# Kernel optimization log

Measured on AMD Instinct MI355X. Metric: run time of the kernel, lower is better.

Reference implementation:

```python
import jax, jax.numpy as jnp
from jax import lax
import numpy as np

KW = 9
PAD = KW // 2  # 4, matches int(kernel_width/2) with stride-1 'same' conv


def _scnn_dir(x, w, b):
    """Sequential SCNN scan over axis 1 of x (shape [N, S, W, C]).
    Each step: cur = relu(conv1d_along_C(prev)) + x[:, i], out[0] = x[:, 0].
    conv is cross-correlation with kernel w (shape [KW]) + scalar bias b,
    matching nn.Conv2d(1, 1, kernel_size=(1, KW), padding=(0, PAD)).
    """
    k = w.reshape(1, 1, 1, KW)  # OIHW-style kernel: out=1, in=1, (1, KW)

    def conv(prev):  # prev: [N, W, C]
        y = lax.conv_general_dilated(prev[:, None, :, :], k,
                                     window_strides=(1, 1),
                                     padding=((0, 0), (PAD, PAD)))
        return y[:, 0] + b  # [N, W, C]

    xt = jnp.moveaxis(x, 1, 0)  # [S, N, W, C]

    def step(prev, xi):
        cur = jax.nn.relu(conv(prev)) + xi
        return cur, cur

    _, rest = lax.scan(step, xt[0], xt[1:])
    out = jnp.concatenate([xt[:1], rest], axis=0)
    return jnp.moveaxis(out, 0, 1)  # [N, S, W, C]


def setup_inputs() -> dict:
    key = jax.random.key(0)
    ks = jax.random.split(key, 9)
    N, C, H, W = 8, 128, 160, 160
    x = jax.random.normal(ks[0], (N, C, H, W), dtype=jnp.float32)
    scale = 1.0 / np.sqrt(KW)  # torch Conv2d default init scale (uniform bound)
    def wgt(k):
        return jax.random.uniform(k, (KW,), jnp.float32, -scale, scale)
    def bia(k):
        return jax.random.uniform(k, (), jnp.float32, -scale, scale)
    return {
        "x": x,
        "w_d": wgt(ks[1]), "b_d": bia(ks[2]),
        "w_u": wgt(ks[3]), "b_u": bia(ks[4]),
        "w_l": wgt(ks[5]), "b_l": bia(ks[6]),
        "w_r": wgt(ks[7]), "b_r": bia(ks[8]),
    }


def reference(x, w_d, b_d, w_u, b_u, w_l, b_l, w_r, b_r):
    out = jnp.transpose(x, (0, 2, 3, 1))                 # NCHW -> NHWC, scan over H (down)
    out = jax.nn.relu(_scnn_dir(out, w_d, b_d))
    out = jnp.flip(out, axis=1)                          # up direction
    out = jax.nn.relu(_scnn_dir(out, w_u, b_u))
    out = jnp.transpose(out, (0, 2, 1, 3))               # scan over W (left)
    out = jax.nn.relu(_scnn_dir(out, w_l, b_l))
    out = jnp.flip(out, axis=1)                          # right direction
    out = jax.nn.relu(_scnn_dir(out, w_r, b_r))
    return jnp.transpose(out, (0, 3, 2, 1))              # back to NCHW
```

## Files before the change

kernel.cpp:

```cpp
#include <hip/hip_runtime.h>

#define NB 8
#define CH 128
#define HH 160
#define WW 160
#define SPILL 100
#define LDS_ROWS 60

__device__ __forceinline__ float dpp_up1(float x) {
    return __int_as_float(__builtin_amdgcn_update_dpp(0, __float_as_int(x), 0x138, 0xF, 0xF, true));
}
__device__ __forceinline__ float dpp_dn1(float x) {
    return __int_as_float(__builtin_amdgcn_update_dpp(0, __float_as_int(x), 0x130, 0xF, 0xF, true));
}

__device__ __forceinline__ float2 conv9(float2 p, const float* w, float b) {
    float m1x = dpp_up1(p.x), m1y = dpp_up1(p.y);
    float m2x = dpp_up1(m1x), m2y = dpp_up1(m1y);
    float p1x = dpp_dn1(p.x), p1y = dpp_dn1(p.y);
    float p2x = dpp_dn1(p1x), p2y = dpp_dn1(p1y);
    float e0=m2x,e1=m2y,e2=m1x,e3=m1y,e4=p.x,e5=p.y,e6=p1x,e7=p1y,e8=p2x,e9=p2y;
    float ax = fmaf(w[0], e0, b);       ax = fmaf(w[3], e3, ax); ax = fmaf(w[6], e6, ax);
    float bx = w[1]*e1;                 bx = fmaf(w[4], e4, bx); bx = fmaf(w[7], e7, bx);
    float cx = w[2]*e2;                 cx = fmaf(w[5], e5, cx); cx = fmaf(w[8], e8, cx);
    float ay = fmaf(w[0], e1, b);       ay = fmaf(w[3], e4, ay); ay = fmaf(w[6], e7, ay);
    float by = w[1]*e2;                 by = fmaf(w[4], e5, by); by = fmaf(w[7], e8, by);
    float cy = w[2]*e3;                 cy = fmaf(w[5], e6, cy); cy = fmaf(w[8], e9, cy);
    return make_float2((ax + bx) + cx, (ay + by) + cy);
}

__global__ __launch_bounds__(256) void k0_transpose(const float* __restrict__ x,
                                                    float* __restrict__ A) {
    __shared__ float t[32][132];
    int p0 = blockIdx.x * 128;
    int c0 = blockIdx.y * 32;
    int n  = blockIdx.z;
    int tid = threadIdx.x;
    const float* xn = x + (size_t)n * CH * HH * WW;
    float* An = A + (size_t)n * HH * WW * CH;
    #pragma unroll
    for (int j = 0; j < 4; j++) {
        int c = j*8 + tid/32;
        int q4 = (tid%32)*4;
        float4 v = *(const float4*)(xn + (size_t)(c0 + c) * (HH*WW) + p0 + q4);
        *(float4*)&t[c][q4] = v;
    }
    __syncthreads();
    #pragma unroll
    for (int j = 0; j < 8; j++) {
        int p  = j*16 + tid/16;
        int cq = (tid%16)*2;
        float2 v = make_float2(t[cq][p], t[cq+1][p]);
        *(float2*)(An + (size_t)(p0 + p) * CH + c0 + cq) = v;
    }
}

__global__ __launch_bounds__(64) void k1_vert(float* __restrict__ A,
        const float* __restrict__ wdp, const float* __restrict__ bdp,
        const float* __restrict__ wup, const float* __restrict__ bup) {
    __shared__ float lds[LDS_ROWS][CH];
    int lane = threadIdx.x;
    int w = blockIdx.x, n = blockIdx.y;
    float wd[9], wu[9];
    #pragma unroll
    for (int j = 0; j < 9; j++) { wd[j] = wdp[j]; wu[j] = wup[j]; }
    float bd = bdp[0], bu = bup[0];
    float* col = A + ((size_t)n * HH * WW + w) * CH + 2*lane;
    const size_t RS = (size_t)WW * CH;

    float2 d;
    float2 qf[16];
    #pragma unroll
    for (int i = 0; i < 16; i++) qf[i] = *(const float2*)(col + (size_t)i * RS);
    for (int hb = 0; hb < HH; hb += 16) {
        #pragma unroll
        for (int k = 0; k < 16; k++) {
            int h = hb + k;
            float2 xr = qf[k];
            if (h + 16 < HH) qf[k] = *(const float2*)(col + (size_t)(h+16) * RS);
            if (h == 0) d = xr;
            else {
                float2 cv = conv9(d, wd, bd);
                d.x = fmaxf(cv.x, 0.f) + xr.x;
                d.y = fmaxf(cv.y, 0.f) + xr.y;
            }
            float rx = fmaxf(d.x, 0.f), ry = fmaxf(d.y, 0.f);
            if (h < SPILL) *(float2*)(col + (size_t)h * RS) = make_float2(rx, ry);
            else { lds[h-SPILL][lane] = rx; lds[h-SPILL][64+lane] = ry; }
        }
    }

    float2 u;
    float2 tf[16];
    #pragma unroll
    for (int k = 0; k < 16; k++) {
        int h = HH - 1 - k;
        tf[k] = make_float2(lds[h-SPILL][lane], lds[h-SPILL][64+lane]);
    }
    for (int sb = 0; sb < HH; sb += 16) {
        #pragma unroll
        for (int k = 0; k < 16; k++) {
            int s = sb + k;
            int h = HH - 1 - s;
            float2 t2 = tf[k];
            int h2 = h - 16;
            if (h2 >= SPILL)    tf[k] = make_float2(lds[h2-SPILL][lane], lds[h2-SPILL][64+lane]);
            else if (h2 >= 0)   tf[k] = *(const float2*)(col + (size_t)h2 * RS);
            if (s == 0) u = t2;
            else {
                float2 cv = conv9(u, wu, bu);
                u.x = fmaxf(cv.x, 0.f) + t2.x;
                u.y = fmaxf(cv.y, 0.f) + t2.y;
            }
            *(float2*)(col + (size_t)h * RS) = u;
        }
    }
}

__global__ __launch_bounds__(64) void k2_horz(float* __restrict__ A,
        const float* __restrict__ wlp, const float* __restrict__ blp,
        const float* __restrict__ wrp, const float* __restrict__ brp,
        float* __restrict__ out) {
    __shared__ float lds[LDS_ROWS][CH];
    int lane = threadIdx.x;
    int hp = blockIdx.x, n = blockIdx.y;
    float wl[9], wr[9];
    #pragma unroll
    for (int j = 0; j < 9; j++) { wl[j] = wlp[j]; wr[j] = wrp[j]; }
    float bl = blp[0], br = brp[0];
    float* row0 = A + ((size_t)n * HH + hp) * WW * CH + 2*lane;
    const size_t PS = CH;

    float2 l;
    float2 qf[16];
    #pragma unroll
    for (int i = 0; i < 16; i++) qf[i] = *(const float2*)(row0 + (size_t)i * PS);
    for (int ab = 0; ab < WW; ab += 16) {
        #pragma unroll
        for (int k = 0; k < 16; k++) {
            int a = ab + k;
            float2 xr = qf[k];
            if (a + 16 < WW) qf[k] = *(const float2*)(row0 + (size_t)(a+16) * PS);
            xr.x = fmaxf(xr.x, 0.f); xr.y = fmaxf(xr.y, 0.f);
            if (a == 0) l = xr;
            else {
                float2 cv = conv9(l, wl, bl);
                l.x = fmaxf(cv.x, 0.f) + xr.x;
                l.y = fmaxf(cv.y, 0.f) + xr.y;
            }
            float rx = fmaxf(l.x, 0.f), ry = fmaxf(l.y, 0.f);
            if (a < SPILL) *(float2*)(row0 + (size_t)a * PS) = make_float2(rx, ry);
            else {
                int r = a - SPILL;
                int sw = r & 31;
                lds[r][lane ^ sw] = rx;
                lds[r][64 + (lane ^ sw)] = ry;
            }
        }
    }

    float2 u;
    float2 tf[16];
    #pragma unroll
    for (int k = 0; k < 16; k++) {
        int a = WW - 1 - k;
        int r = a - SPILL;
        int sw = r & 31;
        tf[k] = make_float2(lds[r][lane ^ sw], lds[r][64 + (lane ^ sw)]);
    }
    int ho  = HH - 1 - hp;
    int l31 = lane & 31;
    int hi  = lane >> 5;
    float* ob = out + ((size_t)(n * CH + hi) * HH + ho) * WW + l31;
    int jf = (179 - l31) % 60;
    int js = 59;

    for (int sb = 0; sb < WW; sb += 32) {
        #pragma unroll
        for (int kk = 0; kk < 32; kk++) {
            int s = sb + kk;
            int a = WW - 1 - s;
            float2 t6 = tf[kk & 15];
            int a2 = a - 16;
            if (a2 >= SPILL) {
                int r = a2 - SPILL;
                int sw = r & 31;
                tf[kk & 15] = make_float2(lds[r][lane ^ sw], lds[r][64 + (lane ^ sw)]);
            } else if (a2 >= 0) {
                tf[kk & 15] = *(const float2*)(row0 + (size_t)a2 * PS);
            }
            if (s == 0) u = t6;
            else {
                float2 cv = conv9(u, wr, br);
                u.x = fmaxf(cv.x, 0.f) + t6.x;
                u.y = fmaxf(cv.y, 0.f) + t6.y;
            }
            {
                int sw = js & 31;
                lds[js][lane ^ sw]        = fmaxf(u.x, 0.f);
                lds[js][64 + (lane ^ sw)] = fmaxf(u.y, 0.f);
            }
            js = js ? js - 1 : 59;
        }
        {
            int jx = jf & 31;
            int pl = jf * 128 + (hi << 6);
            const float* lp = &lds[0][0];
            #pragma unroll
            for (int i = 0; i < 64; i++) {
                float v = lp[pl + (i ^ jx)];
                ob[(size_t)(2*i) * (HH*WW) + sb] = v;
            }
            jf -= 32; if (jf < 0) jf += 60;
        }
    }
}

extern "C" void kernel_launch(void* const* d_in, const int* in_sizes, int n_in,
                              void* d_out, int out_size, void* d_ws, size_t ws_size,
                              hipStream_t stream) {
    (void)in_sizes; (void)n_in; (void)out_size; (void)ws_size;
    const float* x  = (const float*)d_in[0];
    const float* wd = (const float*)d_in[1];
    const float* bd = (const float*)d_in[2];
    const float* wu = (const float*)d_in[3];
    const float* bu = (const float*)d_in[4];
    const float* wl = (const float*)d_in[5];
    const float* bl = (const float*)d_in[6];
    const float* wr = (const float*)d_in[7];
    const float* br = (const float*)d_in[8];
    float* out = (float*)d_out;
    float* A   = (float*)d_ws;

    dim3 g0(HH*WW/128, CH/32, NB), b0(256);
    k0_transpose<<<g0, b0, 0, stream>>>(x, A);

    dim3 g1(WW, NB), b1(64);
    k1_vert<<<g1, b1, 0, stream>>>(A, wd, bd, wu, bu);

    dim3 g2(HH, NB);
    k2_horz<<<g2, b1, 0, stream>>>(A, wl, bl, wr, br, out);
}
```

Baseline: 332.1 us.

## Keep middle scan rows in registers, last rows in LDS to cut global traffic

Both scan kernels now keep rows 48-95 of the first-direction result in a 48-entry register array, rows 96-159 in a 64-row LDS buffer, and write only rows 0-47 to global memory. The reverse scan reads the register and LDS rows directly instead of round-tripping them through global memory, and prefetches the global rows it still needs. k2 reuses the LDS rows in place for the output transpose, with fixed flush points. Launch bounds now request two waves per SIMD, so the extra register pressure may cause spills or lower occupancy.

```diff
diff --git a/kernel.cpp b/kernel.cpp
--- a/kernel.cpp
+++ b/kernel.cpp
@@ -4,8 +4,6 @@
 #define CH 128
 #define HH 160
 #define WW 160
-#define SPILL 100
-#define LDS_ROWS 60
 
 __device__ __forceinline__ float dpp_up1(float x) {
     return __int_as_float(__builtin_amdgcn_update_dpp(0, __float_as_int(x), 0x138, 0xF, 0xF, true));
@@ -29,6 +27,12 @@
     return make_float2((ax + bx) + cx, (ay + by) + cy);
 }
 
+__device__ __forceinline__ void scan_step(float2& st, float2 xr, const float* w, float b) {
+    float2 cv = conv9(st, w, b);
+    st.x = fmaxf(cv.x, 0.f) + xr.x;
+    st.y = fmaxf(cv.y, 0.f) + xr.y;
+}
+
 __global__ __launch_bounds__(256) void k0_transpose(const float* __restrict__ x,
                                                     float* __restrict__ A) {
     __shared__ float t[32][132];
@@ -55,10 +59,10 @@
     }
 }
 
-__global__ __launch_bounds__(64) void k1_vert(float* __restrict__ A,
+__global__ __launch_bounds__(64, 2) void k1_vert(float* __restrict__ A,
         const float* __restrict__ wdp, const float* __restrict__ bdp,
         const float* __restrict__ wup, const float* __restrict__ bup) {
-    __shared__ float lds[LDS_ROWS][CH];
+    __shared__ float lds[64][CH];
     int lane = threadIdx.x;
     int w = blockIdx.x, n = blockIdx.y;
     float wd[9], wu[9];
@@ -69,149 +73,216 @@
     const size_t RS = (size_t)WW * CH;
 
     float2 d;
+    float2 rr[48];
     float2 qf[16];
     #pragma unroll
     for (int i = 0; i < 16; i++) qf[i] = *(const float2*)(col + (size_t)i * RS);
-    for (int hb = 0; hb < HH; hb += 16) {
+
+    for (int hb = 0; hb < 48; hb += 16) {
         #pragma unroll
         for (int k = 0; k < 16; k++) {
             int h = hb + k;
             float2 xr = qf[k];
+            qf[k] = *(const float2*)(col + (size_t)(h+16) * RS);
+            if (h == 0) d = xr;
+            else scan_step(d, xr, wd, bd);
+            *(float2*)(col + (size_t)h * RS) = make_float2(fmaxf(d.x,0.f), fmaxf(d.y,0.f));
+        }
+    }
+    #pragma unroll
+    for (int seg = 0; seg < 3; seg++) {
+        #pragma unroll
+        for (int k = 0; k < 16; k++) {
+            int h = 48 + seg*16 + k;
+            float2 xr = qf[k];
+            qf[k] = *(const float2*)(col + (size_t)(h+16) * RS);
+            scan_step(d, xr, wd, bd);
+            rr[seg*16 + k] = make_float2(fmaxf(d.x,0.f), fmaxf(d.y,0.f));
+        }
+    }
+    for (int hb = 96; hb < 160; hb += 16) {
+        #pragma unroll
+        for (int k = 0; k < 16; k++) {
+            int h = hb + k;
+            float2 xr = qf[k];
             if (h + 16 < HH) qf[k] = *(const float2*)(col + (size_t)(h+16) * RS);
-            if (h == 0) d = xr;
-            else {
-                float2 cv = conv9(d, wd, bd);
-                d.x = fmaxf(cv.x, 0.f) + xr.x;
-                d.y = fmaxf(cv.y, 0.f) + xr.y;
-            }
-            float rx = fmaxf(d.x, 0.f), ry = fmaxf(d.y, 0.f);
-            if (h < SPILL) *(float2*)(col + (size_t)h * RS) = make_float2(rx, ry);
-            else { lds[h-SPILL][lane] = rx; lds[h-SPILL][64+lane] = ry; }
+            scan_step(d, xr, wd, bd);
+            lds[h-96][lane]    = fmaxf(d.x,0.f);
+            lds[h-96][64+lane] = fmaxf(d.y,0.f);
         }
     }
 
     float2 u;
-    float2 tf[16];
-    #pragma unroll
-    for (int k = 0; k < 16; k++) {
-        int h = HH - 1 - k;
-        tf[k] = make_float2(lds[h-SPILL][lane], lds[h-SPILL][64+lane]);
-    }
-    for (int sb = 0; sb < HH; sb += 16) {
-        #pragma unroll
-        for (int k = 0; k < 16; k++) {
-            int s = sb + k;
-            int h = HH - 1 - s;
-            float2 t2 = tf[k];
+    float2 gq[16];
+    for (int sb = 0; sb < 64; sb += 16) {
+        #pragma unroll
+        for (int k = 0; k < 16; k++) {
+            int s = sb + k, h = 159 - s, r = h - 96;
+            float2 t2 = make_float2(lds[r][lane], lds[r][64+lane]);
+            if (sb == 0 && k == 0) u = t2;
+            else scan_step(u, t2, wu, bu);
+            *(float2*)(col + (size_t)h * RS) = u;
+        }
+    }
+    #pragma unroll
+    for (int seg = 0; seg < 3; seg++) {
+        #pragma unroll
+        for (int k = 0; k < 16; k++) {
+            int h = 95 - seg*16 - k;
+            float2 t2 = rr[h - 48];
+            scan_step(u, t2, wu, bu);
+            *(float2*)(col + (size_t)h * RS) = u;
+            if (seg == 0) gq[k] = *(const float2*)(col + (size_t)(47-k) * RS);
+        }
+    }
+    for (int sb = 112; sb < 160; sb += 16) {
+        #pragma unroll
+        for (int k = 0; k < 16; k++) {
+            int s = sb + k, h = 159 - s;
+            float2 t2 = gq[k];
             int h2 = h - 16;
-            if (h2 >= SPILL)    tf[k] = make_float2(lds[h2-SPILL][lane], lds[h2-SPILL][64+lane]);
-            else if (h2 >= 0)   tf[k] = *(const float2*)(col + (size_t)h2 * RS);
-            if (s == 0) u = t2;
-            else {
-                float2 cv = conv9(u, wu, bu);
-                u.x = fmaxf(cv.x, 0.f) + t2.x;
-                u.y = fmaxf(cv.y, 0.f) + t2.y;
-            }
+            if (h2 >= 0) gq[k] = *(const float2*)(col + (size_t)h2 * RS);
+            scan_step(u, t2, wu, bu);
             *(float2*)(col + (size_t)h * RS) = u;
         }
     }
 }
 
-__global__ __launch_bounds__(64) void k2_horz(float* __restrict__ A,
+__global__ __launch_bounds__(64, 2) void k2_horz(float* __restrict__ A,
         const float* __restrict__ wlp, const float* __restrict__ blp,
         const float* __restrict__ wrp, const float* __restrict__ brp,
         float* __restrict__ out) {
-    __shared__ float lds[LDS_ROWS][CH];
+    __shared__ float lds[64][CH];
     int lane = threadIdx.x;
     int hp = blockIdx.x, n = blockIdx.y;
-    float wl[9], wr[9];
-    #pragma unroll
-    for (int j = 0; j < 9; j++) { wl[j] = wlp[j]; wr[j] = wrp[j]; }
-    float bl = blp[0], br = brp[0];
+    float wA[9], wB[9];
+    #pragma unroll
+    for (int j = 0; j < 9; j++) { wA[j] = wlp[j]; wB[j] = wrp[j]; }
+    float bA = blp[0], bB = brp[0];
     float* row0 = A + ((size_t)n * HH + hp) * WW * CH + 2*lane;
     const size_t PS = CH;
 
     float2 l;
+    float2 rr[48];
     float2 qf[16];
     #pragma unroll
     for (int i = 0; i < 16; i++) qf[i] = *(const float2*)(row0 + (size_t)i * PS);
-    for (int ab = 0; ab < WW; ab += 16) {
+
+    for (int ab = 0; ab < 48; ab += 16) {
+        #pragma unroll
+        for (int k = 0; k < 16; k++) {
+            int a = ab + k;
+            float2 xr = qf[k];
+            qf[k] = *(const float2*)(row0 + (size_t)(a+16) * PS);
+            xr.x = fmaxf(xr.x, 0.f); xr.y = fmaxf(xr.y, 0.f);
+            if (a == 0) l = xr;
+            else scan_step(l, xr, wA, bA);
+            *(float2*)(row0 + (size_t)a * PS) = make_float2(fmaxf(l.x,0.f), fmaxf(l.y,0.f));
+        }
+    }
+    #pragma unroll
+    for (int seg = 0; seg < 3; seg++) {
+        #pragma unroll
+        for (int k = 0; k < 16; k++) {
+            int a = 48 + seg*16 + k;
+            float2 xr = qf[k];
+            qf[k] = *(const float2*)(row0 + (size_t)(a+16) * PS);
+            xr.x = fmaxf(xr.x, 0.f); xr.y = fmaxf(xr.y, 0.f);
+            scan_step(l, xr, wA, bA);
+            rr[seg*16 + k] = make_float2(fmaxf(l.x,0.f), fmaxf(l.y,0.f));
+        }
+    }
+    for (int ab = 96; ab < 160; ab += 16) {
         #pragma unroll
         for (int k = 0; k < 16; k++) {
             int a = ab + k;
             float2 xr = qf[k];
             if (a + 16 < WW) qf[k] = *(const float2*)(row0 + (size_t)(a+16) * PS);
             xr.x = fmaxf(xr.x, 0.f); xr.y = fmaxf(xr.y, 0.f);
-            if (a == 0) l = xr;
-            else {
-                float2 cv = conv9(l, wl, bl);
-                l.x = fmaxf(cv.x, 0.f) + xr.x;
-                l.y = fmaxf(cv.y, 0.f) + xr.y;
-            }
-            float rx = fmaxf(l.x, 0.f), ry = fmaxf(l.y, 0.f);
-            if (a < SPILL) *(float2*)(row0 + (size_t)a * PS) = make_float2(rx, ry);
-            else {
-                int r = a - SPILL;
-                int sw = r & 31;
-                lds[r][lane ^ sw] = rx;
-                lds[r][64 + (lane ^ sw)] = ry;
-            }
+            scan_step(l, xr, wA, bA);
+            int r = a - 96, sw = r & 31;
+            lds[r][lane ^ sw]        = fmaxf(l.x,0.f);
+            lds[r][64 + (lane ^ sw)] = fmaxf(l.y,0.f);
         }
     }
 
     float2 u;
-    float2 tf[16];
-    #pragma unroll
-    for (int k = 0; k < 16; k++) {
-        int a = WW - 1 - k;
-        int r = a - SPILL;
-        int sw = r & 31;
-        tf[k] = make_float2(lds[r][lane ^ sw], lds[r][64 + (lane ^ sw)]);
-    }
+    float2 gq[16];
     int ho  = HH - 1 - hp;
     int l31 = lane & 31;
     int hi  = lane >> 5;
     float* ob = out + ((size_t)(n * CH + hi) * HH + ho) * WW + l31;
-    int jf = (179 - l31) % 60;
-    int js = 59;
-
-    for (int sb = 0; sb < WW; sb += 32) {
-        #pragma unroll
-        for (int kk = 0; kk < 32; kk++) {
-            int s = sb + kk;
-            int a = WW - 1 - s;
-            float2 t6 = tf[kk & 15];
+    int jx = 31 - l31;
+    const float* lp = &lds[0][0];
+
+    for (int sb = 0; sb < 64; sb += 16) {
+        #pragma unroll
+        for (int k = 0; k < 16; k++) {
+            int s = sb + k, r = 63 - s, sw = r & 31;
+            int ci = lane ^ sw;
+            float2 t2 = make_float2(lds[r][ci], lds[r][64+ci]);
+            if (sb == 0 && k == 0) u = t2;
+            else scan_step(u, t2, wB, bB);
+            lds[r][ci]    = fmaxf(u.x, 0.f);
+            lds[r][64+ci] = fmaxf(u.y, 0.f);
+        }
+        if (sb == 16 || sb == 48) {
+            int jf = (sb == 16 ? 63 : 31) - l31;
+            int pl = jf*128 + (hi << 6);
+            int so = sb - 16;
+            #pragma unroll
+            for (int i = 0; i < 64; i++)
+                ob[(size_t)(2*i) * (HH*WW) + so] = lp[pl + (i ^ jx)];
+        }
+    }
+    #pragma unroll
+    for (int seg = 0; seg < 3; seg++) {
+        #pragma unroll
+        for (int k = 0; k < 16; k++) {
+            int s = 64 + seg*16 + k;
+            int a = 159 - s;
+            float2 t2 = rr[a - 48];
+            scan_step(u, t2, wB, bB);
+            int js = 63 - 16*seg - k;
+            int sw = js & 31;
+            lds[js][lane ^ sw]        = fmaxf(u.x, 0.f);
+            lds[js][64 + (lane ^ sw)] = fmaxf(u.y, 0.f);
+            if (seg == 0) gq[k] = *(const float2*)(row0 + (size_t)(47-k) * PS);
+        }
+        if (seg == 1) {
+            int jf = 63 - l31;
+            int pl = jf*128 + (hi << 6);
+            #pragma unroll
+            for (int i = 0; i < 64; i++)
+                ob[(size_t)(2*i) * (HH*WW) + 64] = lp[pl + (i ^ jx)];
+        }
+    }
+    for (int sb = 112; sb < 160; sb += 16) {
+        #pragma unroll
+        for (int k = 0; k < 16; k++) {
+            int s = sb + k, a = 159 - s;
+            float2 t2 = gq[k];
             int a2 = a - 16;
-            if (a2 >= SPILL) {
-                int r = a2 - SPILL;
-                int sw = r & 31;
-                tf[kk & 15] = make_float2(lds[r][lane ^ sw], lds[r][64 + (lane ^ sw)]);
-            } else if (a2 >= 0) {
-                tf[kk & 15] = *(const float2*)(row0 + (size_t)a2 * PS);
-            }
-            if (s == 0) u = t6;
-            else {
-                float2 cv = conv9(u, wr, br);
-                u.x = fmaxf(cv.x, 0.f) + t6.x;
-                u.y = fmaxf(cv.y, 0.f) + t6.y;
-            }
-            {
-                int sw = js & 31;
-                lds[js][lane ^ sw]        = fmaxf(u.x, 0.f);
-                lds[js][64 + (lane ^ sw)] = fmaxf(u.y, 0.f);
-            }
-            js = js ? js - 1 : 59;
-        }
-        {
-            int jx = jf & 31;
-            int pl = jf * 128 + (hi << 6);
-            const float* lp = &lds[0][0];
+            if (a2 >= 0) gq[k] = *(const float2*)(row0 + (size_t)a2 * PS);
+            scan_step(u, t2, wB, bB);
+            int js = 63 - (s & 63);
+            int sw = js & 31;
+            lds[js][lane ^ sw]        = fmaxf(u.x, 0.f);
+            lds[js][64 + (lane ^ sw)] = fmaxf(u.y, 0.f);
+        }
+        if (sb == 112) {
+            int jf = 31 - l31;
+            int pl = jf*128 + (hi << 6);
             #pragma unroll
-            for (int i = 0; i < 64; i++) {
-                float v = lp[pl + (i ^ jx)];
-                ob[(size_t)(2*i) * (HH*WW) + sb] = v;
-            }
-            jf -= 32; if (jf < 0) jf += 60;
+            for (int i = 0; i < 64; i++)
+                ob[(size_t)(2*i) * (HH*WW) + 96] = lp[pl + (i ^ jx)];
+        }
+        if (sb == 144) {
+            int jf = 63 - l31;
+            int pl = jf*128 + (hi << 6);
+            #pragma unroll
+            for (int i = 0; i < 64; i++)
+                ob[(size_t)(2*i) * (HH*WW) + 128] = lp[pl + (i ^ jx)];
         }
     }
 }
```

Result: slower. 593.3 us (+78.6%).

## Split vertical scan channels across two wavefronts with LDS halo exchange

Applied to the files above, without the earlier changes.

The vertical (down/up) scan kernel now uses 128 threads, one channel per thread across two wavefronts, instead of 64 threads each holding two channels. The 9-tap convolution across the wavefront boundary is completed with a small double-buffered LDS halo of 4 values per side, which needs a __syncthreads every row. The intent is to shorten the per-step serial dependency chain and double parallelism in the latency-bound sequential scan. The cost is a block-wide barrier on every one of the 320 steps, plus extra LDS traffic.

```diff
diff --git a/kernel.cpp b/kernel.cpp
--- a/kernel.cpp
+++ b/kernel.cpp
@@ -29,6 +29,15 @@
     return make_float2((ax + bx) + cx, (ay + by) + cy);
 }
 
+__device__ __forceinline__ float conv9s(float p, const float* w, float b) {
+    float m1=dpp_up1(p), m2=dpp_up1(m1), m3=dpp_up1(m2), m4=dpp_up1(m3);
+    float q1=dpp_dn1(p), q2=dpp_dn1(q1), q3=dpp_dn1(q2), q4=dpp_dn1(q3);
+    float a = fmaf(w[0], m4, b); a = fmaf(w[3], m1, a); a = fmaf(w[6], q2, a);
+    float c = w[1]*m3;           c = fmaf(w[4], p,  c); c = fmaf(w[7], q3, c);
+    float e = w[2]*m2;           e = fmaf(w[5], q1, e); e = fmaf(w[8], q4, e);
+    return (a + c) + e;
+}
+
 __global__ __launch_bounds__(256) void k0_transpose(const float* __restrict__ x,
                                                     float* __restrict__ A) {
     __shared__ float t[32][132];
@@ -55,64 +64,89 @@
     }
 }
 
-__global__ __launch_bounds__(64) void k1_vert(float* __restrict__ A,
+__global__ __launch_bounds__(128) void k1_vert(float* __restrict__ A,
         const float* __restrict__ wdp, const float* __restrict__ bdp,
         const float* __restrict__ wup, const float* __restrict__ bup) {
     __shared__ float lds[LDS_ROWS][CH];
-    int lane = threadIdx.x;
+    __shared__ float halo[2][8];
+    int tid  = threadIdx.x;
+    int lane = tid & 63;
+    int wid  = tid >> 6;
+    int ch   = tid;
     int w = blockIdx.x, n = blockIdx.y;
     float wd[9], wu[9];
     #pragma unroll
     for (int j = 0; j < 9; j++) { wd[j] = wdp[j]; wu[j] = wup[j]; }
     float bd = bdp[0], bu = bup[0];
-    float* col = A + ((size_t)n * HH * WW + w) * CH + 2*lane;
+
+    float wsD[4], wsU[4];
+    #pragma unroll
+    for (int j = 0; j < 4; j++) {
+        float a = 0.f, b2 = 0.f;
+        if (wid == 0) { int t = lane - 60; if (t >= 0 && j <= t) { a = wdp[8-t+j]; b2 = wup[8-t+j]; } }
+        else          { if (lane < 4 && j >= lane)              { a = wdp[j-lane]; b2 = wup[j-lane]; } }
+        wsD[j] = a; wsU[j] = b2;
+    }
+    bool pub  = (wid == 0) ? (lane >= 60) : (lane < 4);
+    int hslot = (wid == 0) ? (lane - 60) : (4 + lane);
+    int hoff  = wid ? 0 : 4;
+
+    float* col = A + ((size_t)n * HH * WW + w) * CH + ch;
     const size_t RS = (size_t)WW * CH;
 
-    float2 d;
-    float2 qf[16];
-    #pragma unroll
-    for (int i = 0; i < 16; i++) qf[i] = *(const float2*)(col + (size_t)i * RS);
+    float d;
+    float qf[16];
+    #pragma unroll
+    for (int i = 0; i < 16; i++) qf[i] = col[(size_t)i * RS];
+    int par = 0;
     for (int hb = 0; hb < HH; hb += 16) {
         #pragma unroll
         for (int k = 0; k < 16; k++) {
             int h = hb + k;
-            float2 xr = qf[k];
-            if (h + 16 < HH) qf[k] = *(const float2*)(col + (size_t)(h+16) * RS);
+            float xr = qf[k];
+            if (h + 16 < HH) qf[k] = col[(size_t)(h+16) * RS];
             if (h == 0) d = xr;
             else {
-                float2 cv = conv9(d, wd, bd);
-                d.x = fmaxf(cv.x, 0.f) + xr.x;
-                d.y = fmaxf(cv.y, 0.f) + xr.y;
-            }
-            float rx = fmaxf(d.x, 0.f), ry = fmaxf(d.y, 0.f);
-            if (h < SPILL) *(float2*)(col + (size_t)h * RS) = make_float2(rx, ry);
-            else { lds[h-SPILL][lane] = rx; lds[h-SPILL][64+lane] = ry; }
-        }
-    }
-
-    float2 u;
-    float2 tf[16];
-    #pragma unroll
-    for (int k = 0; k < 16; k++) {
-        int h = HH - 1 - k;
-        tf[k] = make_float2(lds[h-SPILL][lane], lds[h-SPILL][64+lane]);
-    }
+                float4 hv = *(const float4*)&halo[par][hoff];
+                float cv = conv9s(d, wd, bd);
+                cv = fmaf(wsD[0], hv.x, cv); cv = fmaf(wsD[1], hv.y, cv);
+                cv = fmaf(wsD[2], hv.z, cv); cv = fmaf(wsD[3], hv.w, cv);
+                d = fmaxf(cv, 0.f) + xr;
+                par ^= 1;
+            }
+            if (pub) halo[par][hslot] = d;
+            __syncthreads();
+            float rd = fmaxf(d, 0.f);
+            if (h < SPILL) col[(size_t)h * RS] = rd;
+            else           lds[h-SPILL][ch] = rd;
+        }
+    }
+
+    float u;
+    float tf[16];
+    #pragma unroll
+    for (int k = 0; k < 16; k++) tf[k] = lds[59 - k][ch];
     for (int sb = 0; sb < HH; sb += 16) {
         #pragma unroll
         for (int k = 0; k < 16; k++) {
             int s = sb + k;
             int h = HH - 1 - s;
-            float2 t2 = tf[k];
+            float t2 = tf[k];
             int h2 = h - 16;
-            if (h2 >= SPILL)    tf[k] = make_float2(lds[h2-SPILL][lane], lds[h2-SPILL][64+lane]);
-            else if (h2 >= 0)   tf[k] = *(const float2*)(col + (size_t)h2 * RS);
+            if (h2 >= SPILL)    tf[k] = lds[h2-SPILL][ch];
+            else if (h2 >= 0)   tf[k] = col[(size_t)h2 * RS];
             if (s == 0) u = t2;
             else {
-                float2 cv = conv9(u, wu, bu);
-                u.x = fmaxf(cv.x, 0.f) + t2.x;
-                u.y = fmaxf(cv.y, 0.f) + t2.y;
-            }
-            *(float2*)(col + (size_t)h * RS) = u;
+                float4 hv = *(const float4*)&halo[par][hoff];
+                float cv = conv9s(u, wu, bu);
+                cv = fmaf(wsU[0], hv.x, cv); cv = fmaf(wsU[1], hv.y, cv);
+                cv = fmaf(wsU[2], hv.z, cv); cv = fmaf(wsU[3], hv.w, cv);
+                u = fmaxf(cv, 0.f) + t2;
+                par ^= 1;
+            }
+            if (pub) halo[par][hslot] = u;
+            __syncthreads();
+            col[(size_t)h * RS] = u;
         }
     }
 }
@@ -235,9 +269,9 @@
     dim3 g0(HH*WW/128, CH/32, NB), b0(256);
     k0_transpose<<<g0, b0, 0, stream>>>(x, A);
 
-    dim3 g1(WW, NB), b1(64);
+    dim3 g1(WW, NB), b1(128);
     k1_vert<<<g1, b1, 0, stream>>>(A, wd, bd, wu, bu);
 
-    dim3 g2(HH, NB);
-    k2_horz<<<g2, b1, 0, stream>>>(A, wl, bl, wr, br, out);
-}
+    dim3 g2(HH, NB), b2(64);
+    k2_horz<<<g2, b2, 0, stream>>>(A, wl, bl, wr, br, out);
+}
```

Result: slower. 396.7 us (+19.4%).
